# Kernel tuning notes

Hardware: AMD Instinct MI355X
Metric: run time of the kernel (lower is better)

## Reference

```python
import jax, jax.numpy as jnp
import numpy as np

N = 100000   # total nodes
E = 600000   # total edges
B = 50       # graphs in batch
F = 40       # functions per graph (guaranteed by construction)
NPG = N // B # nodes per graph
TF = B * F   # total functions
D0 = 64; H = 128; C = 2
INTER_STEPS = 2


def _seg_mean(x, ids, n):
    s = jax.ops.segment_sum(x, ids, num_segments=n)
    c = jax.ops.segment_sum(jnp.ones((ids.shape[0], 1), x.dtype), ids, num_segments=n)
    return s / jnp.maximum(c, 1.0)


def _enc_edge(h, Ws, Wn, b, src, dst):
    # 2-layer message-passing encoder: h = relu(W_self h + W_nbr mean_{j->i} h_j + b)
    for l in range(2):
        agg = _seg_mean(h[src], dst, h.shape[0])
        h = jax.nn.relu(h @ Ws[l] + agg @ Wn[l] + b[l])
    return h


def _enc_plain(h, Ws, b):
    # encoder on a scale with empty edge set: neighbor term is zero
    for l in range(2):
        h = jax.nn.relu(h @ Ws[l] + b[l])
    return h


def _forward(x0, Wp, bp, e0in_Ws, e0in_Wn, e0in_b, e1in_Ws, e1in_b, e2in_Ws, e2in_b,
             enc0_Ws, enc0_Wn, enc0_b, enc1_Ws, enc1_b, enc2_Ws, enc2_b,
             A0, A1, A2, U0, U1, D1, D2, ib0, ib1, ib2, H1, hb1, H2, hb2,
             edge_index, b0, assign0_local):
    src, dst = edge_index[0], edge_index[1]
    # every graph has exactly F functions, so cumsum offsets reduce to b0*F
    assign0 = assign0_local + b0 * F
    assign1 = jnp.arange(TF, dtype=jnp.int32) // F
    h0 = jax.nn.relu(x0 @ Wp + bp)  # dropout = identity at eval
    h1 = jnp.zeros((TF, H), x0.dtype)
    h2 = jnp.zeros((B, H), x0.dtype)
    h0 = _enc_edge(h0, e0in_Ws, e0in_Wn, e0in_b, src, dst)
    h1 = _enc_plain(h1, e1in_Ws, e1in_b)
    h2 = _enc_plain(h2, e2in_Ws, e2in_b)
    for _ in range(INTER_STEPS):
        # inter-scale fusion: pool up (scatter-mean), broadcast down (gather)
        p01 = _seg_mean(h0, assign0, TF)   # node -> function
        p12 = _seg_mean(h1, assign1, B)    # function -> graph
        n0 = jax.nn.relu(h0 @ A0 + h1[assign0] @ D1 + ib0)
        n1 = jax.nn.relu(h1 @ A1 + p01 @ U0 + h2[assign1] @ D2 + ib1)
        n2 = jax.nn.relu(h2 @ A2 + p12 @ U1 + ib2)
        h0, h1, h2 = n0, n1, n2
        h0 = _enc_edge(h0, enc0_Ws, enc0_Wn, enc0_b, src, dst)
        h1 = _enc_plain(h1, enc1_Ws, enc1_b)
        h2 = _enc_plain(h2, enc2_Ws, enc2_b)
    g0 = _seg_mean(h0, b0, B)        # global_mean_pool over nodes
    g1 = _seg_mean(h1, assign1, B)   # mean over functions per graph
    g = jnp.concatenate([g0, g1, h2], axis=-1)  # [B, 3H]
    return jax.nn.relu(g @ H1 + hb1) @ H2 + hb2


def setup_inputs() -> dict:
    key = jax.random.key(0)
    ks = iter(jax.random.split(key, 64))
    def W(*shape):
        return jax.random.normal(next(ks), shape, dtype=jnp.float32) * 0.05
    inp = {}
    inp["x0"] = jax.random.normal(next(ks), (N, D0), dtype=jnp.float32)
    inp["edge_index"] = jax.random.randint(next(ks), (2, E), 0, N, dtype=jnp.int32)
    inp["b0"] = (jnp.arange(N, dtype=jnp.int32) // NPG)            # sorted graph ids
    inp["assign0_local"] = (jnp.arange(N, dtype=jnp.int32) % NPG) % F  # all F ids per graph
    inp["Wp"] = W(D0, H); inp["bp"] = jnp.zeros((H,), jnp.float32)
    for name in ["e0in", "enc0"]:
        inp[name + "_Ws"] = W(2, H, H); inp[name + "_Wn"] = W(2, H, H)
        inp[name + "_b"] = jnp.zeros((2, H), jnp.float32)
    for name in ["e1in", "e2in", "enc1", "enc2"]:
        inp[name + "_Ws"] = W(2, H, H)
        inp[name + "_b"] = jnp.zeros((2, H), jnp.float32)
    for nm in ["A0", "A1", "A2", "U0", "U1", "D1", "D2"]:
        inp[nm] = W(H, H)
    for nm in ["ib0", "ib1", "ib2"]:
        inp[nm] = jnp.zeros((H,), jnp.float32)
    inp["H1"] = W(3 * H, H); inp["hb1"] = jnp.zeros((H,), jnp.float32)
    inp["H2"] = W(H, C); inp["hb2"] = jnp.zeros((C,), jnp.float32)
    return inp


def reference(x0, edge_index, b0, assign0_local, Wp, bp,
              e0in_Ws, e0in_Wn, e0in_b, e1in_Ws, e1in_b, e2in_Ws, e2in_b,
              enc0_Ws, enc0_Wn, enc0_b, enc1_Ws, enc1_b, enc2_Ws, enc2_b,
              A0, A1, A2, U0, U1, D1, D2, ib0, ib1, ib2, H1, hb1, H2, hb2):
    return _forward(x0, Wp, bp, e0in_Ws, e0in_Wn, e0in_b, e1in_Ws, e1in_b,
                    e2in_Ws, e2in_b, enc0_Ws, enc0_Wn, enc0_b, enc1_Ws, enc1_b,
                    enc2_Ws, enc2_b, A0, A1, A2, U0, U1, D1, D2, ib0, ib1, ib2,
                    H1, hb1, H2, hb2, edge_index, b0, assign0_local)
```

## Files before the change

kernel.cpp:

```cpp
#include <hip/hip_runtime.h>

namespace {

constexpr int N   = 100000;
constexpr int E   = 600000;
constexpr int B   = 50;
constexpr int F   = 40;
constexpr int TF  = B * F;
constexpr int D0  = 64;
constexpr int H   = 128;
constexpr int C   = 2;

typedef __attribute__((ext_vector_type(8))) __bf16 bf16x8;
typedef __attribute__((ext_vector_type(8))) unsigned short us8;
typedef __attribute__((ext_vector_type(4))) float f32x4;

__device__ __forceinline__ float asf(unsigned u) { return __uint_as_float(u); }
__device__ __forceinline__ unsigned bfr(float x) {
  unsigned u = __float_as_uint(x);
  return (u + 0x7FFFu + ((u >> 16) & 1u)) >> 16;
}

__device__ __forceinline__ void glds16(const void* g, void* l) {
  __builtin_amdgcn_global_load_lds(
      (const __attribute__((address_space(1))) unsigned*)g,
      (__attribute__((address_space(3))) unsigned*)l, 16, 0, 0);
}


__global__ void hist_edges(const int* __restrict__ dst, int* __restrict__ deg) {
  int e = blockIdx.x * 256 + threadIdx.x;
  if (e < E) atomicAdd(&deg[dst[e]], 1);
}

__global__ void hist_nodes(const int* __restrict__ b0, const int* __restrict__ a0l,
                           int* __restrict__ cnt1, int* __restrict__ assign0) {
  __shared__ int lh[TF];
  int t = threadIdx.x;
  for (int j = t; j < TF; j += 256) lh[j] = 0;
  __syncthreads();
  int i = blockIdx.x * 256 + t;
  if (i < N) {
    int g = b0[i];
    int a = g * F + a0l[i];
    assign0[i] = a;
    atomicAdd(&lh[a], 1);
  }
  __syncthreads();
  for (int j = t; j < TF; j += 256) {
    int c = lh[j];
    if (c) atomicAdd(&cnt1[j], c);
  }
}

__global__ void scan1(const int* __restrict__ cnt, int* __restrict__ offs,
                      int* __restrict__ part) {
  __shared__ int lds[256];
  int t = threadIdx.x;
  int base = blockIdx.x * 1024 + t * 4;
  int v[4];
#pragma unroll
  for (int j = 0; j < 4; ++j) v[j] = (base + j < N) ? cnt[base + j] : 0;
  int s = v[0] + v[1] + v[2] + v[3];
  lds[t] = s;
  __syncthreads();
  for (int off = 1; off < 256; off <<= 1) {
    int x = (t >= off) ? lds[t - off] : 0;
    __syncthreads();
    lds[t] += x;
    __syncthreads();
  }
  int ex = lds[t] - s;
  if (t == 255) part[blockIdx.x] = lds[255];
  int run = ex;
#pragma unroll
  for (int j = 0; j < 4; ++j) {
    if (base + j < N) offs[base + j] = run;
    run += v[j];
  }
}

__global__ void scan2(const int* __restrict__ part, int* __restrict__ partEx, int nb) {
  __shared__ int lds[128];
  int t = threadIdx.x;
  int s = (t < nb) ? part[t] : 0;
  lds[t] = s;
  __syncthreads();
  for (int off = 1; off < 128; off <<= 1) {
    int x = (t >= off) ? lds[t - off] : 0;
    __syncthreads();
    lds[t] += x;
    __syncthreads();
  }
  partEx[t] = lds[t] - s;
}

__global__ void scan3(int* __restrict__ offs, const int* __restrict__ partEx,
                      const int* __restrict__ deg, float* __restrict__ rdeg,
                      const int* __restrict__ cnt1, float* __restrict__ rdeg1,
                      float* __restrict__ rdegB) {
  int i = blockIdx.x * 256 + threadIdx.x;
  if (i < N) {
    offs[i] += partEx[i >> 10];
    rdeg[i] = 1.0f / fmaxf((float)deg[i], 1.0f);
    if (i == 0) offs[N] = E;
    if (i < TF) rdeg1[i] = 1.0f / fmaxf((float)cnt1[i], 1.0f);
    if (i < B) {
      int s = 0;
      for (int f = 0; f < F; ++f) s += cnt1[i * F + f];
      rdegB[i] = 1.0f / fmaxf((float)s, 1.0f);
    }
  }
}

__global__ void scatter_k(const int* __restrict__ src, const int* __restrict__ dst,
                          const int* __restrict__ offs, int* __restrict__ cursor,
                          int* __restrict__ srcS) {
  int e = blockIdx.x * 256 + threadIdx.x;
  if (e < E) {
    int d = dst[e];
    int pos = offs[d] + atomicAdd(&cursor[d], 1);
    srcS[pos] = src[e];
  }
}

struct WPtrs { const float* w[19]; };
__global__ void conv_w(WPtrs wp, unsigned short* __restrict__ wt) {
  int i = blockIdx.x >> 6;
  int e = (blockIdx.x & 63) * 256 + threadIdx.x;
  int k = e >> 7, c = e & 127;
  float x = wp.w[i][e];
  unsigned h = bfr(x);
  unsigned l = bfr(x - asf(h << 16));
  int cs = (c & 7) * 16 + (c >> 3);
  size_t o = (size_t)i * 32768 + (k >> 5) * 4096 + cs * 32 + (k & 31);
  wt[o] = (unsigned short)h;
  wt[o + 16384] = (unsigned short)l;
}

__global__ void conv_wp(const float* __restrict__ w, unsigned short* __restrict__ wt) {
  int e = blockIdx.x * 256 + threadIdx.x;
  int k = e >> 7, c = e & 127;
  float x = w[e];
  unsigned h = bfr(x);
  unsigned l = bfr(x - asf(h << 16));
  int cs = (c & 7) * 16 + (c >> 3);
  size_t o = (size_t)(k >> 5) * 4096 + cs * 32 + (k & 31);
  wt[o] = (unsigned short)h;
  wt[o + 8192] = (unsigned short)l;
}

__global__ void x0split(const float* __restrict__ x0, unsigned short* __restrict__ xs) {
  int i = blockIdx.x * 256 + threadIdx.x;
  if (i >= N * D0) return;
  int row = i >> 6, c = i & 63;
  float x = x0[i];
  unsigned h = bfr(x);
  unsigned l = bfr(x - asf(h << 16));
  xs[(size_t)row * 128 + c] = (unsigned short)h;
  xs[(size_t)row * 128 + 64 + c] = (unsigned short)l;
}

__global__ void warm_k(const uint4* __restrict__ w, unsigned* __restrict__ dummy) {
  uint4 v = w[blockIdx.x * 256 + threadIdx.x];
  unsigned x = v.x ^ v.y ^ v.z ^ v.w;
  if (x == 0xDEADBEEFu) dummy[0] = 1u;
}

__global__ void agg_k(const unsigned short* __restrict__ Act,
                      const int* __restrict__ offs, const int* __restrict__ srcS,
                      const float* __restrict__ rdeg, unsigned short* __restrict__ Out) {
  int wid = blockIdx.x * 4 + (threadIdx.x >> 6);
  int lane = threadIdx.x & 63;
  if (wid >= N) return;
  int o0 = offs[wid], o1 = offs[wid + 1];
  float s0 = 0.f, s1 = 0.f;
  int e = o0;
  for (; e + 3 < o1; e += 4) {
    unsigned v0 = *(const unsigned*)(Act + (size_t)srcS[e] * 256 + lane * 2);
    unsigned v1 = *(const unsigned*)(Act + (size_t)srcS[e + 1] * 256 + lane * 2);
    unsigned v2 = *(const unsigned*)(Act + (size_t)srcS[e + 2] * 256 + lane * 2);
    unsigned v3 = *(const unsigned*)(Act + (size_t)srcS[e + 3] * 256 + lane * 2);
    s0 += asf(v0 << 16) + asf(v1 << 16) + asf(v2 << 16) + asf(v3 << 16);
    s1 += asf(v0 & 0xFFFF0000u) + asf(v1 & 0xFFFF0000u) +
          asf(v2 & 0xFFFF0000u) + asf(v3 & 0xFFFF0000u);
  }
  for (; e < o1; ++e) {
    unsigned v0 = *(const unsigned*)(Act + (size_t)srcS[e] * 256 + lane * 2);
    s0 += asf(v0 << 16);
    s1 += asf(v0 & 0xFFFF0000u);
  }
  float sc = rdeg[wid];
  unsigned h0 = bfr(s0 * sc), h1 = bfr(s1 * sc);
  *(unsigned*)(Out + (size_t)wid * 256 + lane * 2) = h0 | (h1 << 16);
}

template <int KD, bool AGG, bool GATH, bool BLO = true>
__global__ __launch_bounds__(256, 3)
void mgemm(const unsigned short* __restrict__ Ai, const unsigned short* __restrict__ W1,
           const unsigned short* __restrict__ Bi, const unsigned short* __restrict__ W2,
           const float* __restrict__ Gt, const int* __restrict__ Gidx,
           const float* __restrict__ bias, unsigned short* __restrict__ Oi, int n) {
  __shared__ unsigned short wlds[2][2][4096];
  constexpr int KS = KD / 32;
  constexpr int NS = (AGG ? 2 : 1) * KS;
  constexpr int KLO = KD * 128;
  constexpr int ARS = 2 * KD;
  const int t = threadIdx.x, wv = t >> 6, ln = t & 63;
  const int row0 = blockIdx.x * 128 + wv * 32;
  const int lm = ln & 15, kg = ln >> 4;
  int ar0 = row0 + lm, ar1 = row0 + 16 + lm;
  if (ar0 >= n) ar0 = 0;
  if (ar1 >= n) ar1 = 0;
  const size_t a0off = (size_t)ar0 * ARS, a1off = (size_t)ar1 * ARS;

  f32x4 acc[2][8];
#pragma unroll
  for (int i = 0; i < 2; ++i)
#pragma unroll
    for (int j = 0; j < 8; ++j) acc[i][j] = (f32x4){0.f, 0.f, 0.f, 0.f};

  uint4 sA, sB, sC, sD;
  bf16x8 a0h[2], a0l[2], a1h[2], a1l[2];

  auto ldst = [&](int s) {
    const unsigned short* W = (AGG && s >= KS) ? W2 : W1;
    const unsigned short* ph = W + (s & (KS - 1)) * 4096;
    sA = *(const uint4*)(ph + t * 8);
    sB = *(const uint4*)(ph + 2048 + t * 8);
    sC = *(const uint4*)(ph + KLO + t * 8);
    sD = *(const uint4*)(ph + KLO + 2048 + t * 8);
  };
  auto wrst = [&](int buf) {
    *(uint4*)&wlds[buf][0][t * 8] = sA;
    *(uint4*)&wlds[buf][0][2048 + t * 8] = sB;
    *(uint4*)&wlds[buf][1][t * 8] = sC;
    *(uint4*)&wlds[buf][1][2048 + t * 8] = sD;
  };
  auto loadA = [&](int s, int w) {
    const bool bpass = AGG && (s >= KS);
    const unsigned short* X = bpass ? Bi : Ai;
    int kk = (s & (KS - 1)) * 32 + kg * 8;
    a0h[w] = *(const bf16x8*)(X + a0off + kk);
    a1h[w] = *(const bf16x8*)(X + a1off + kk);
    if (!bpass || BLO) {
      a0l[w] = *(const bf16x8*)(X + a0off + KD + kk);
      a1l[w] = *(const bf16x8*)(X + a1off + KD + kk);
    }
  };

  ldst(0); wrst(0); loadA(0, 0);
  __syncthreads();

#pragma unroll
  for (int s = 0; s < NS; ++s) {
    const int buf = s & 1;
    const bool uselo = !(AGG && (s >= KS)) || BLO;
    if (s + 1 < NS) { ldst(s + 1); loadA(s + 1, buf ^ 1); }
#pragma unroll
    for (int nf = 0; nf < 8; ++nf) {
      const int wo = (nf * 16 + lm) * 32 + kg * 8;
      bf16x8 wh = *(const bf16x8*)&wlds[buf][0][wo];
      bf16x8 wl = *(const bf16x8*)&wlds[buf][1][wo];
      acc[0][nf] = __builtin_amdgcn_mfma_f32_16x16x32_bf16(a0h[buf], wh, acc[0][nf], 0, 0, 0);
      acc[0][nf] = __builtin_amdgcn_mfma_f32_16x16x32_bf16(a0h[buf], wl, acc[0][nf], 0, 0, 0);
      if (uselo)
        acc[0][nf] = __builtin_amdgcn_mfma_f32_16x16x32_bf16(a0l[buf], wh, acc[0][nf], 0, 0, 0);
      acc[1][nf] = __builtin_amdgcn_mfma_f32_16x16x32_bf16(a1h[buf], wh, acc[1][nf], 0, 0, 0);
      acc[1][nf] = __builtin_amdgcn_mfma_f32_16x16x32_bf16(a1h[buf], wl, acc[1][nf], 0, 0, 0);
      if (uselo)
        acc[1][nf] = __builtin_amdgcn_mfma_f32_16x16x32_bf16(a1l[buf], wh, acc[1][nf], 0, 0, 0);
    }
    if (s + 1 < NS) wrst(buf ^ 1);
    __syncthreads();
  }

  float4 bq0 = *(const float4*)&bias[lm * 8];
  float4 bq1 = *(const float4*)&bias[lm * 8 + 4];
  float bsv[8] = {bq0.x, bq0.y, bq0.z, bq0.w, bq1.x, bq1.y, bq1.z, bq1.w};
#pragma unroll
  for (int mf = 0; mf < 2; ++mf)
#pragma unroll
    for (int rr = 0; rr < 4; ++rr) {
      int row = row0 + mf * 16 + kg * 4 + rr;
      if (row >= n) continue;
      float gvv[8];
      if (GATH) {
        const float* grow = Gt + (size_t)Gidx[row] * H + lm * 8;
        float4 g0 = *(const float4*)grow;
        float4 g1 = *(const float4*)(grow + 4);
        gvv[0] = g0.x; gvv[1] = g0.y; gvv[2] = g0.z; gvv[3] = g0.w;
        gvv[4] = g1.x; gvv[5] = g1.y; gvv[6] = g1.z; gvv[7] = g1.w;
      }
      us8 hv, lv;
#pragma unroll
      for (int nf = 0; nf < 8; ++nf) {
        float v = acc[mf][nf][rr] + bsv[nf];
        if (GATH) v += gvv[nf];
        v = fmaxf(v, 0.f);
        unsigned h = bfr(v);
        hv[nf] = (unsigned short)h;
        lv[nf] = (unsigned short)bfr(v - asf(h << 16));
      }
      *(us8*)(Oi + (size_t)row * 256 + lm * 8) = hv;
      *(us8*)(Oi + (size_t)row * 256 + 128 + lm * 8) = lv;
    }
}

template <bool ISH1>
__global__ __launch_bounds__(512)
void fused_chain(const unsigned short* __restrict__ Ai,
                 const float* __restrict__ P, const float* __restrict__ pscale,
                 const float* __restrict__ Gt,
                 const unsigned short* __restrict__ Wd,
                 const unsigned short* __restrict__ Wa,
                 const unsigned short* __restrict__ Wu,
                 const unsigned short* __restrict__ We0,
                 const unsigned short* __restrict__ We1,
                 const float* __restrict__ bn, const float* __restrict__ be0,
                 const float* __restrict__ be1,
                 float* __restrict__ outD, unsigned short* __restrict__ Ao,
                 float* __restrict__ outF, int n) {
  __shared__ unsigned short act[128 * 256];
  __shared__ unsigned short wl[2][16384];
  const int t = threadIdx.x, wv = t >> 6, ln = t & 63;
  const int lm = ln & 15, kg = ln >> 4;
  const int rbase = blockIdx.x * 128 + wv * 16;
  const int lbase = wv * 16;
  int ar = rbase + lm;
  if (ar >= n) ar = 0;

  const unsigned short* mats[5] = {Wd, Wa, Wu, We0, We1};

  f32x4 acc[8];
  auto zacc = [&]() {
#pragma unroll
    for (int nf = 0; nf < 8; ++nf) acc[nf] = (f32x4){0.f, 0.f, 0.f, 0.f};
  };

  auto ldwl = [&](int s, int b) {
    const unsigned short* hi = mats[s >> 1] + (s & 1) * 8192;
    const unsigned short* lo = mats[s >> 1] + 16384 + (s & 1) * 8192;
    const int wo = wv * 1024;
    const int lo8 = ln * 8;
#pragma unroll
    for (int j = 0; j < 2; ++j) {
      glds16(hi + wo + j * 512 + lo8, &wl[b][wo + j * 512]);
      glds16(lo + wo + j * 512 + lo8, &wl[b][8192 + wo + j * 512]);
    }
  };
  auto ldact = [&]() {
    const unsigned short* src = Ai + (size_t)blockIdx.x * (128 * 256);
    const int base = wv * 4096;
    const int lo8 = ln * 8;
#pragma unroll
    for (int j = 0; j < 8; ++j)
      glds16(src + base + j * 512 + lo8, &act[base + j * 512]);
  };

  auto donf = [&](int b, int ksl, bf16x8 ah, bf16x8 al) {
#pragma unroll
    for (int nf = 0; nf < 8; ++nf) {
      const int wo = ksl * 4096 + (nf * 16 + lm) * 32 + kg * 8;
      bf16x8 wh = *(const bf16x8*)&wl[b][wo];
      bf16x8 wq = *(const bf16x8*)&wl[b][8192 + wo];
      acc[nf] = __builtin_amdgcn_mfma_f32_16x16x32_bf16(ah, wh, acc[nf], 0, 0, 0);
      acc[nf] = __builtin_amdgcn_mfma_f32_16x16x32_bf16(ah, wq, acc[nf], 0, 0, 0);
      acc[nf] = __builtin_amdgcn_mfma_f32_16x16x32_bf16(al, wh, acc[nf], 0, 0, 0);
    }
  };

  auto epiAct = [&](const float* bias, bool gath) {
    float4 b0 = *(const float4*)&bias[lm * 8];
    float4 b1 = *(const float4*)&bias[lm * 8 + 4];
    float bv[8] = {b0.x, b0.y, b0.z, b0.w, b1.x, b1.y, b1.z, b1.w};
#pragma unroll
    for (int rr = 0; rr < 4; ++rr) {
      int rl = lbase + kg * 4 + rr;
      int rg = rbase + kg * 4 + rr;
      float gv[8] = {0.f, 0.f, 0.f, 0.f, 0.f, 0.f, 0.f, 0.f};
      if (ISH1 && gath && rg < n) {
        const float* grow = Gt + (size_t)(rg / F) * H + lm * 8;
        float4 g0 = *(const float4*)grow;
        float4 g1 = *(const float4*)(grow + 4);
        gv[0] = g0.x; gv[1] = g0.y; gv[2] = g0.z; gv[3] = g0.w;
        gv[4] = g1.x; gv[5] = g1.y; gv[6] = g1.z; gv[7] = g1.w;
      }
      us8 hv, lv;
#pragma unroll
      for (int nf = 0; nf < 8; ++nf) {
        float v = acc[nf][rr] + bv[nf] + gv[nf];
        v = fmaxf(v, 0.f);
        unsigned h = bfr(v);
        hv[nf] = (unsigned short)h;
        lv[nf] = (unsigned short)bfr(v - asf(h << 16));
      }
      *(us8*)&act[rl * 256 + lm * 8] = hv;
      *(us8*)&act[rl * 256 + 128 + lm * 8] = lv;
    }
  };

  ldact();
  ldwl(0, 0);
  __syncthreads();
  ldwl(1, 1);

#pragma unroll
  for (int s = 0; s < 10; ++s) {
    const int b = s & 1;
    if (s == 0 || s == 2 || s == 6 || s == 8) zacc();
    const int m = s >> 1;
#pragma unroll
    for (int ksl = 0; ksl < 2; ++ksl) {
      const int ks = (s & 1) * 2 + ksl;
      bf16x8 ah, al;
      if (m == 2) {
        const float* pp = P + (size_t)ar * H + ks * 32 + kg * 8;
        float4 f0 = *(const float4*)pp;
        float4 f1 = *(const float4*)(pp + 4);
        if (ISH1) {
          float sc = pscale[ar];
          f0.x *= sc; f0.y *= sc; f0.z *= sc; f0.w *= sc;
          f1.x *= sc; f1.y *= sc; f1.z *= sc; f1.w *= sc;
        }
        float fv[8] = {f0.x, f0.y, f0.z, f0.w, f1.x, f1.y, f1.z, f1.w};
        us8 h8, l8;
#pragma unroll
        for (int j = 0; j < 8; ++j) {
          unsigned h = bfr(fv[j]);
          h8[j] = (unsigned short)h;
          l8[j] = (unsigned short)bfr(fv[j] - asf(h << 16));
        }
        ah = __builtin_bit_cast(bf16x8, h8);
        al = __builtin_bit_cast(bf16x8, l8);
      } else {
        int rl = lbase + lm;
        ah = *(const bf16x8*)&act[rl * 256 + ks * 32 + kg * 8];
        al = *(const bf16x8*)&act[rl * 256 + 128 + ks * 32 + kg * 8];
      }
      donf(b, ksl, ah, al);
    }
    if (s == 1) {
#pragma unroll
      for (int rr = 0; rr < 4; ++rr) {
        int rg = rbase + kg * 4 + rr;
        if (rg < n) {
          float* op = outD + (size_t)rg * H + lm * 8;
          *(float4*)op = make_float4(acc[0][rr], acc[1][rr], acc[2][rr], acc[3][rr]);
          *(float4*)(op + 4) = make_float4(acc[4][rr], acc[5][rr], acc[6][rr], acc[7][rr]);
        }
      }
    }
    if (s == 5) epiAct(bn, true);
    if (s == 7) epiAct(be0, false);
    if (s == 9) {
      float4 b0 = *(const float4*)&be1[lm * 8];
      float4 b1 = *(const float4*)&be1[lm * 8 + 4];
      float bv[8] = {b0.x, b0.y, b0.z, b0.w, b1.x, b1.y, b1.z, b1.w};
#pragma unroll
      for (int rr = 0; rr < 4; ++rr) {
        int rg = rbase + kg * 4 + rr;
        if (rg >= n) continue;
        us8 hv, lv;
        float fv[8];
#pragma unroll
        for (int nf = 0; nf < 8; ++nf) {
          float v = fmaxf(acc[nf][rr] + bv[nf], 0.f);
          fv[nf] = v;
          unsigned h = bfr(v);
          hv[nf] = (unsigned short)h;
          lv[nf] = (unsigned short)bfr(v - asf(h << 16));
        }
        *(us8*)(Ao + (size_t)rg * 256 + lm * 8) = hv;
        *(us8*)(Ao + (size_t)rg * 256 + 128 + lm * 8) = lv;
        if (outF) {
          float* op = outF + (size_t)rg * H + lm * 8;
          *(float4*)op = make_float4(fv[0], fv[1], fv[2], fv[3]);
          *(float4*)(op + 4) = make_float4(fv[4], fv[5], fv[6], fv[7]);
        }
      }
    }
    if (s + 1 < 10) {
      __syncthreads();
      if (s + 2 < 10) ldwl(s + 2, b);
    }
  }
}

__global__ void init_bcast(const float* __restrict__ Ws1, const float* __restrict__ b1,
                           const float* __restrict__ Ws2, const float* __restrict__ b2,
                           unsigned short* __restrict__ h1i, unsigned short* __restrict__ h2i) {
  __shared__ float z0[128];
  int t = threadIdx.x;
  bool ish2 = (blockIdx.x == 20);
  const float* W = ish2 ? Ws2 : Ws1;
  const float* bb = ish2 ? b2 : b1;
  z0[t] = fmaxf(bb[t], 0.f);
  __syncthreads();
  float s = bb[128 + t];
  for (int k = 0; k < 128; ++k) s += z0[k] * W[16384 + k * 128 + t];
  s = fmaxf(s, 0.f);
  unsigned h = bfr(s);
  unsigned l = bfr(s - asf(h << 16));
  if (ish2) {
    for (int r = 0; r < B; ++r) {
      h2i[(size_t)r * 256 + t] = (unsigned short)h;
      h2i[(size_t)r * 256 + 128 + t] = (unsigned short)l;
    }
  } else {
    int r0 = blockIdx.x * 100;
    for (int r = 0; r < 100; ++r) {
      h1i[(size_t)(r0 + r) * 256 + t] = (unsigned short)h;
      h1i[(size_t)(r0 + r) * 256 + 128 + t] = (unsigned short)l;
    }
  }
}

__global__ void pool_p01(const unsigned short* __restrict__ Act,
                         const int* __restrict__ a0l, const int* __restrict__ b0,
                         float* __restrict__ p01s) {
  __shared__ float acc[F][H];
  int t = threadIdx.x;
#pragma unroll
  for (int f = 0; f < F; ++f) acc[f][t] = 0.f;
  int rowbase = blockIdx.x * 250;
  for (int i = 0; i < 250; ++i) {
    size_t r = (size_t)(rowbase + i) * 256 + t;
    acc[a0l[rowbase + i]][t] += asf((unsigned)Act[r] << 16) + asf((unsigned)Act[r + 128] << 16);
  }
  int g = b0[rowbase];
#pragma unroll
  for (int f = 0; f < F; ++f)
    atomicAdd(&p01s[((size_t)(g * F + f)) * H + t], acc[f][t]);
}

__global__ void pool_g0(const unsigned short* __restrict__ Act,
                        const int* __restrict__ b0, float* __restrict__ g0s) {
  int t = threadIdx.x;
  int rowbase = blockIdx.x * 250;
  float a = 0.f;
  for (int i = 0; i < 250; ++i) {
    size_t r = (size_t)(rowbase + i) * 256 + t;
    a += asf((unsigned)Act[r] << 16) + asf((unsigned)Act[r + 128] << 16);
  }
  atomicAdd(&g0s[(size_t)b0[rowbase] * H + t], a);
}

__global__ void mean40i(const unsigned short* __restrict__ Act, float* __restrict__ outp) {
  int t = threadIdx.x, g = blockIdx.x;
  float a = 0.f;
  for (int i = 0; i < F; ++i) {
    size_t r = (size_t)(g * F + i) * 256 + t;
    a += asf((unsigned)Act[r] << 16) + asf((unsigned)Act[r + 128] << 16);
  }
  outp[(size_t)g * H + t] = a * (1.0f / F);
}

__global__ void head_k(const float* __restrict__ g0s, const float* __restrict__ rdegB,
                       const float* __restrict__ g1, const float* __restrict__ h2,
                       const float* __restrict__ W1h, const float* __restrict__ b1h,
                       const float* __restrict__ W2h, const float* __restrict__ b2h,
                       float* __restrict__ out) {
  __shared__ float gv[3 * H];
  __shared__ float z[H];
  int b = blockIdx.x, t = threadIdx.x;
  gv[t] = g0s[(size_t)b * H + t] * rdegB[b];
  gv[H + t] = g1[(size_t)b * H + t];
  gv[2 * H + t] = h2[(size_t)b * H + t];
  __syncthreads();
  float s = b1h[t];
  for (int k = 0; k < 3 * H; ++k) s += gv[k] * W1h[k * H + t];
  z[t] = fmaxf(s, 0.f);
  __syncthreads();
  if (t < C) {
    float o = b2h[t];
    for (int k = 0; k < H; ++k) o += z[k] * W2h[k * C + t];
    out[b * C + t] = o;
  }
}

}

extern "C" void kernel_launch(void* const* d_in, const int* in_sizes, int n_in,
                              void* d_out, int out_size, void* d_ws, size_t ws_size,
                              hipStream_t stream) {
  (void)in_sizes; (void)n_in; (void)out_size; (void)ws_size;
  const float* x0   = (const float*)d_in[0];
  const int*   ei   = (const int*)d_in[1];
  const int*   src  = ei;
  const int*   dst  = ei + E;
  const int*   b0   = (const int*)d_in[2];
  const int*   a0l  = (const int*)d_in[3];
  const float* Wp   = (const float*)d_in[4];
  const float* bp   = (const float*)d_in[5];
  const float* e0in_Ws = (const float*)d_in[6];
  const float* e0in_Wn = (const float*)d_in[7];
  const float* e0in_b  = (const float*)d_in[8];
  const float* enc0_Ws = (const float*)d_in[9];
  const float* enc0_Wn = (const float*)d_in[10];
  const float* enc0_b  = (const float*)d_in[11];
  const float* e1in_Ws = (const float*)d_in[12];
  const float* e1in_b  = (const float*)d_in[13];
  const float* e2in_Ws = (const float*)d_in[14];
  const float* e2in_b  = (const float*)d_in[15];
  const float* enc1_Ws = (const float*)d_in[16];
  const float* enc1_b  = (const float*)d_in[17];
  const float* enc2_Ws = (const float*)d_in[18];
  const float* enc2_b  = (const float*)d_in[19];
  const float* A0 = (const float*)d_in[20];
  const float* A1 = (const float*)d_in[21];
  const float* A2 = (const float*)d_in[22];
  const float* U0 = (const float*)d_in[23];
  const float* U1 = (const float*)d_in[24];
  const float* D1 = (const float*)d_in[25];
  const float* D2 = (const float*)d_in[26];
  const float* ib0 = (const float*)d_in[27];
  const float* ib1 = (const float*)d_in[28];
  const float* ib2 = (const float*)d_in[29];
  const float* H1w = (const float*)d_in[30];
  const float* hb1 = (const float*)d_in[31];
  const float* H2w = (const float*)d_in[32];
  const float* hb2 = (const float*)d_in[33];
  float* out = (float*)d_out;

  char* p = (char*)d_ws;
  auto carve = [&](size_t bytes) {
    char* r = p;
    p += (bytes + 255) & ~(size_t)255;
    return r;
  };
  char* z0 = p;
  int*   deg    = (int*)carve((size_t)N * 4);
  int*   cursor = (int*)carve((size_t)N * 4);
  int*   cnt1   = (int*)carve((size_t)TF * 4);
  float* g0s    = (float*)carve((size_t)B * H * 4);
  size_t zbytes = (size_t)(p - z0);
  unsigned short* h0i  = (unsigned short*)carve((size_t)N * 256 * 2);
  unsigned short* aggi = (unsigned short*)carve((size_t)N * 256 * 2);
  unsigned short* h1a  = (unsigned short*)carve((size_t)2048 * 256 * 2);
  unsigned short* h2ai = (unsigned short*)carve((size_t)128 * 256 * 2);
  float* h1d  = (float*)carve((size_t)TF * H * 4);
  float* h2d  = (float*)carve((size_t)64 * H * 4);
  float* h2f  = (float*)carve((size_t)B * H * 4);
  float* p01s = (float*)carve((size_t)TF * H * 4);
  float* p12  = (float*)carve((size_t)64 * H * 4);
  float* g1   = (float*)carve((size_t)B * H * 4);
  float* rdeg = (float*)carve((size_t)N * 4);
  float* rdeg1 = (float*)carve((size_t)TF * 4);
  float* rdegB = (float*)carve(64 * 4);
  int* offs    = (int*)carve((size_t)(N + 64) * 4);
  int* srcS    = (int*)carve((size_t)E * 4);
  int* part    = (int*)carve(128 * 4);
  int* partEx  = (int*)carve(128 * 4);
  int* assign0 = (int*)carve((size_t)N * 4);
  unsigned short* wt  = (unsigned short*)carve((size_t)19 * 32768 * 2);
  unsigned short* wt9 = (unsigned short*)carve((size_t)16384 * 2);
  unsigned short* xs  = aggi;

  const int HH = H * H;
  const int MG = (N + 127) / 128;

  hipMemsetAsync(z0, 0, zbytes, stream);
  hist_edges<<<(E + 255) / 256, 256, 0, stream>>>(dst, deg);
  hist_nodes<<<(N + 255) / 256, 256, 0, stream>>>(b0, a0l, cnt1, assign0);
  const int nb1 = (N + 1023) / 1024;
  scan1<<<nb1, 256, 0, stream>>>(deg, offs, part);
  scan2<<<1, 128, 0, stream>>>(part, partEx, nb1);
  scan3<<<(N + 255) / 256, 256, 0, stream>>>(offs, partEx, deg, rdeg, cnt1, rdeg1,
                                             rdegB);
  scatter_k<<<(E + 255) / 256, 256, 0, stream>>>(src, dst, offs, cursor, srcS);
  {
    WPtrs wp;
    wp.w[0] = e0in_Ws;      wp.w[1] = e0in_Ws + HH;
    wp.w[2] = e0in_Wn;      wp.w[3] = e0in_Wn + HH;
    wp.w[4] = enc0_Ws;      wp.w[5] = enc0_Ws + HH;
    wp.w[6] = enc0_Wn;      wp.w[7] = enc0_Wn + HH;
    wp.w[8] = A0;
    wp.w[9] = D1;           wp.w[10] = A1;
    wp.w[11] = U0;          wp.w[12] = enc1_Ws;   wp.w[13] = enc1_Ws + HH;
    wp.w[14] = D2;          wp.w[15] = A2;
    wp.w[16] = U1;          wp.w[17] = enc2_Ws;   wp.w[18] = enc2_Ws + HH;
    conv_w<<<19 * 64, 256, 0, stream>>>(wp, wt);
  }
  conv_wp<<<32, 256, 0, stream>>>(Wp, wt9);
  x0split<<<(N * D0 + 255) / 256, 256, 0, stream>>>(x0, xs);

  mgemm<64, false, false><<<MG, 256, 0, stream>>>(
      xs, wt9, nullptr, nullptr, nullptr, nullptr, bp, h0i, N);

  auto encEdgeM = [&](int wsIdx, int wnIdx, const float* barr) {
    for (int l = 0; l < 2; ++l) {
      agg_k<<<N / 4, 256, 0, stream>>>(h0i, offs, srcS, rdeg, aggi);
      mgemm<128, true, false, false><<<MG, 256, 0, stream>>>(
          h0i, wt + (size_t)(wsIdx + l) * 32768, aggi,
          wt + (size_t)(wnIdx + l) * 32768, nullptr, nullptr, barr + l * H, h0i, N);
    }
  };

  encEdgeM(0, 2, e0in_b);
  init_bcast<<<21, 128, 0, stream>>>(e1in_Ws, e1in_b, e2in_Ws, e2in_b, h1a, h2ai);

  for (int step = 0; step < 2; ++step) {
    hipMemsetAsync(p01s, 0, (size_t)TF * H * 4, stream);
    pool_p01<<<400, 128, 0, stream>>>(h0i, a0l, b0, p01s);
    mean40i<<<B, 128, 0, stream>>>(h1a, p12);
    warm_k<<<160, 256, 0, stream>>>((const uint4*)(wt + (size_t)9 * 32768),
                                    (unsigned*)cursor);
    fused_chain<false><<<1, 512, 0, stream>>>(
        h2ai, p12, nullptr, nullptr,
        wt + (size_t)14 * 32768, wt + (size_t)15 * 32768, wt + (size_t)16 * 32768,
        wt + (size_t)17 * 32768, wt + (size_t)18 * 32768,
        ib2, enc2_b, enc2_b + H, h2d, h2ai, h2f, B);
    fused_chain<true><<<16, 512, 0, stream>>>(
        h1a, p01s, rdeg1, h2d,
        wt + (size_t)9 * 32768, wt + (size_t)10 * 32768, wt + (size_t)11 * 32768,
        wt + (size_t)12 * 32768, wt + (size_t)13 * 32768,
        ib1, enc1_b, enc1_b + H, h1d, h1a, nullptr, TF);
    mgemm<128, false, true><<<MG, 256, 0, stream>>>(
        h0i, wt + (size_t)8 * 32768, nullptr, nullptr, h1d, assign0, ib0, h0i, N);
    encEdgeM(4, 6, enc0_b);
  }

  pool_g0<<<400, 128, 0, stream>>>(h0i, b0, g0s);
  mean40i<<<B, 128, 0, stream>>>(h1a, g1);
  head_k<<<B, 128, 0, stream>>>(g0s, rdegB, g1, h2f, H1w, hb1, H2w, hb2, out);
}
```

Baseline: 831.1 us.

## Merge graph-level and function-level fused chains into one launch

The two per-step fused_chain launches (one block for the graph level, 16 blocks for the function level) are replaced by a single 17-block kernel. One block handles the graph-level role and computes h2·D2 for the next step into a double buffer. The first h2·D2 is precomputed by a new small kernel before the loop. This removes the serial dependency and one launch per step so both levels run concurrently. The cost is that the step loops are no longer unrolled and the kernel branches on role.

```diff
diff --git a/kernel.cpp b/kernel.cpp
--- a/kernel.cpp
+++ b/kernel.cpp
@@ -307,30 +307,91 @@
     }
 }
 
-template <bool ISH1>
 __global__ __launch_bounds__(512)
-void fused_chain(const unsigned short* __restrict__ Ai,
-                 const float* __restrict__ P, const float* __restrict__ pscale,
-                 const float* __restrict__ Gt,
-                 const unsigned short* __restrict__ Wd,
-                 const unsigned short* __restrict__ Wa,
-                 const unsigned short* __restrict__ Wu,
-                 const unsigned short* __restrict__ We0,
-                 const unsigned short* __restrict__ We1,
-                 const float* __restrict__ bn, const float* __restrict__ be0,
-                 const float* __restrict__ be1,
-                 float* __restrict__ outD, unsigned short* __restrict__ Ao,
-                 float* __restrict__ outF, int n) {
+void h2d_k(const unsigned short* __restrict__ h2ai, const unsigned short* __restrict__ Wm,
+           float* __restrict__ h2d) {
+  __shared__ unsigned short wl[32768];
+  const int t = threadIdx.x, wv = t >> 6, ln = t & 63;
+  const int lm = ln & 15, kg = ln >> 4;
+  const int lo8 = ln * 8;
+#pragma unroll
+  for (int j = 0; j < 8; ++j)
+    glds16(Wm + (wv * 8 + j) * 512 + lo8, &wl[(wv * 8 + j) * 512]);
+  __syncthreads();
+  if (wv >= 4) return;
+  int ar = wv * 16 + lm;
+  if (ar >= B) ar = 0;
+  f32x4 acc[8];
+#pragma unroll
+  for (int nf = 0; nf < 8; ++nf) acc[nf] = (f32x4){0.f, 0.f, 0.f, 0.f};
+#pragma unroll
+  for (int ks = 0; ks < 4; ++ks) {
+    bf16x8 ah = *(const bf16x8*)(h2ai + (size_t)ar * 256 + ks * 32 + kg * 8);
+    bf16x8 al = *(const bf16x8*)(h2ai + (size_t)ar * 256 + 128 + ks * 32 + kg * 8);
+#pragma unroll
+    for (int nf = 0; nf < 8; ++nf) {
+      const int wo = ks * 4096 + (nf * 16 + lm) * 32 + kg * 8;
+      bf16x8 wh = *(const bf16x8*)&wl[wo];
+      bf16x8 wq = *(const bf16x8*)&wl[16384 + wo];
+      acc[nf] = __builtin_amdgcn_mfma_f32_16x16x32_bf16(ah, wh, acc[nf], 0, 0, 0);
+      acc[nf] = __builtin_amdgcn_mfma_f32_16x16x32_bf16(ah, wq, acc[nf], 0, 0, 0);
+      acc[nf] = __builtin_amdgcn_mfma_f32_16x16x32_bf16(al, wh, acc[nf], 0, 0, 0);
+    }
+  }
+#pragma unroll
+  for (int rr = 0; rr < 4; ++rr) {
+    int rg = wv * 16 + kg * 4 + rr;
+    if (rg < B) {
+      float* op = h2d + (size_t)rg * H + lm * 8;
+      *(float4*)op = make_float4(acc[0][rr], acc[1][rr], acc[2][rr], acc[3][rr]);
+      *(float4*)(op + 4) = make_float4(acc[4][rr], acc[5][rr], acc[6][rr], acc[7][rr]);
+    }
+  }
+}
+
+struct ChainArgs {
+  const unsigned short* Ai1; const unsigned short* Ai2;
+  const float* P1; const float* P2; const float* ps1;
+  const float* Gt1;
+  const unsigned short* w1[5];
+  const unsigned short* w2[6];
+  const float *bn1, *be01, *be11, *bn2, *be02, *be12;
+  float* outD1;
+  unsigned short* Ao1; unsigned short* Ao2;
+  float* outF2;
+  float* outDn2;
+  int n1, n2;
+};
+
+__global__ __launch_bounds__(512)
+void fused_chain2(ChainArgs a) {
   __shared__ unsigned short act[128 * 256];
   __shared__ unsigned short wl[2][16384];
+  const bool role = (blockIdx.x == 16);
   const int t = threadIdx.x, wv = t >> 6, ln = t & 63;
   const int lm = ln & 15, kg = ln >> 4;
-  const int rbase = blockIdx.x * 128 + wv * 16;
+  const int rbase = (role ? 0 : blockIdx.x * 128) + wv * 16;
   const int lbase = wv * 16;
+  const int n = role ? a.n2 : a.n1;
+  const int nst = role ? 12 : 10;
+  const unsigned short* Ai = role ? a.Ai2 : a.Ai1;
+  const float* P = role ? a.P2 : a.P1;
+  unsigned short* Ao = role ? a.Ao2 : a.Ao1;
+  const float* bn  = role ? a.bn2 : a.bn1;
+  const float* be0 = role ? a.be02 : a.be01;
+  const float* be1 = role ? a.be12 : a.be11;
   int ar = rbase + lm;
   if (ar >= n) ar = 0;
 
-  const unsigned short* mats[5] = {Wd, Wa, Wu, We0, We1};
+  const unsigned short* mats[6];
+  if (role) {
+#pragma unroll
+    for (int i = 0; i < 6; ++i) mats[i] = a.w2[i];
+  } else {
+#pragma unroll
+    for (int i = 0; i < 5; ++i) mats[i] = a.w1[i];
+    mats[5] = a.w1[0];
+  }
 
   f32x4 acc[8];
   auto zacc = [&]() {
@@ -350,7 +411,7 @@
     }
   };
   auto ldact = [&]() {
-    const unsigned short* src = Ai + (size_t)blockIdx.x * (128 * 256);
+    const unsigned short* src = Ai + (size_t)(role ? 0 : blockIdx.x) * (128 * 256);
     const int base = wv * 4096;
     const int lo8 = ln * 8;
 #pragma unroll
@@ -379,8 +440,8 @@
       int rl = lbase + kg * 4 + rr;
       int rg = rbase + kg * 4 + rr;
       float gv[8] = {0.f, 0.f, 0.f, 0.f, 0.f, 0.f, 0.f, 0.f};
-      if (ISH1 && gath && rg < n) {
-        const float* grow = Gt + (size_t)(rg / F) * H + lm * 8;
+      if (!role && gath && rg < n) {
+        const float* grow = a.Gt1 + (size_t)(rg / F) * H + lm * 8;
         float4 g0 = *(const float4*)grow;
         float4 g1 = *(const float4*)(grow + 4);
         gv[0] = g0.x; gv[1] = g0.y; gv[2] = g0.z; gv[3] = g0.w;
@@ -405,12 +466,10 @@
   __syncthreads();
   ldwl(1, 1);
 
-#pragma unroll
-  for (int s = 0; s < 10; ++s) {
+  for (int s = 0; s < nst; ++s) {
     const int b = s & 1;
-    if (s == 0 || s == 2 || s == 6 || s == 8) zacc();
+    if ((s & 1) == 0 && s != 4) zacc();
     const int m = s >> 1;
-#pragma unroll
     for (int ksl = 0; ksl < 2; ++ksl) {
       const int ks = (s & 1) * 2 + ksl;
       bf16x8 ah, al;
@@ -418,8 +477,8 @@
         const float* pp = P + (size_t)ar * H + ks * 32 + kg * 8;
         float4 f0 = *(const float4*)pp;
         float4 f1 = *(const float4*)(pp + 4);
-        if (ISH1) {
-          float sc = pscale[ar];
+        if (!role) {
+          float sc = a.ps1[ar];
           f0.x *= sc; f0.y *= sc; f0.z *= sc; f0.w *= sc;
           f1.x *= sc; f1.y *= sc; f1.z *= sc; f1.w *= sc;
         }
@@ -440,12 +499,12 @@
       }
       donf(b, ksl, ah, al);
     }
-    if (s == 1) {
+    if (s == 1 && !role) {
 #pragma unroll
       for (int rr = 0; rr < 4; ++rr) {
         int rg = rbase + kg * 4 + rr;
         if (rg < n) {
-          float* op = outD + (size_t)rg * H + lm * 8;
+          float* op = a.outD1 + (size_t)rg * H + lm * 8;
           *(float4*)op = make_float4(acc[0][rr], acc[1][rr], acc[2][rr], acc[3][rr]);
           *(float4*)(op + 4) = make_float4(acc[4][rr], acc[5][rr], acc[6][rr], acc[7][rr]);
         }
@@ -459,8 +518,8 @@
       float bv[8] = {b0.x, b0.y, b0.z, b0.w, b1.x, b1.y, b1.z, b1.w};
 #pragma unroll
       for (int rr = 0; rr < 4; ++rr) {
+        int rl = lbase + kg * 4 + rr;
         int rg = rbase + kg * 4 + rr;
-        if (rg >= n) continue;
         us8 hv, lv;
         float fv[8];
 #pragma unroll
@@ -471,18 +530,35 @@
           hv[nf] = (unsigned short)h;
           lv[nf] = (unsigned short)bfr(v - asf(h << 16));
         }
-        *(us8*)(Ao + (size_t)rg * 256 + lm * 8) = hv;
-        *(us8*)(Ao + (size_t)rg * 256 + 128 + lm * 8) = lv;
-        if (outF) {
-          float* op = outF + (size_t)rg * H + lm * 8;
-          *(float4*)op = make_float4(fv[0], fv[1], fv[2], fv[3]);
-          *(float4*)(op + 4) = make_float4(fv[4], fv[5], fv[6], fv[7]);
+        if (role) {
+          *(us8*)&act[rl * 256 + lm * 8] = hv;
+          *(us8*)&act[rl * 256 + 128 + lm * 8] = lv;
+        }
+        if (rg < n) {
+          *(us8*)(Ao + (size_t)rg * 256 + lm * 8) = hv;
+          *(us8*)(Ao + (size_t)rg * 256 + 128 + lm * 8) = lv;
+          if (role) {
+            float* op = a.outF2 + (size_t)rg * H + lm * 8;
+            *(float4*)op = make_float4(fv[0], fv[1], fv[2], fv[3]);
+            *(float4*)(op + 4) = make_float4(fv[4], fv[5], fv[6], fv[7]);
+          }
         }
       }
     }
-    if (s + 1 < 10) {
+    if (s == 11) {
+#pragma unroll
+      for (int rr = 0; rr < 4; ++rr) {
+        int rg = rbase + kg * 4 + rr;
+        if (rg < n) {
+          float* op = a.outDn2 + (size_t)rg * H + lm * 8;
+          *(float4*)op = make_float4(acc[0][rr], acc[1][rr], acc[2][rr], acc[3][rr]);
+          *(float4*)(op + 4) = make_float4(acc[4][rr], acc[5][rr], acc[6][rr], acc[7][rr]);
+        }
+      }
+    }
+    if (s + 1 < nst) {
       __syncthreads();
-      if (s + 2 < 10) ldwl(s + 2, b);
+      if (s + 2 < nst) ldwl(s + 2, b);
     }
   }
 }
@@ -640,7 +716,8 @@
   unsigned short* h1a  = (unsigned short*)carve((size_t)2048 * 256 * 2);
   unsigned short* h2ai = (unsigned short*)carve((size_t)128 * 256 * 2);
   float* h1d  = (float*)carve((size_t)TF * H * 4);
-  float* h2d  = (float*)carve((size_t)64 * H * 4);
+  float* h2dA = (float*)carve((size_t)64 * H * 4);
+  float* h2dB = (float*)carve((size_t)64 * H * 4);
   float* h2f  = (float*)carve((size_t)B * H * 4);
   float* p01s = (float*)carve((size_t)TF * H * 4);
   float* p12  = (float*)carve((size_t)64 * H * 4);
@@ -699,23 +776,35 @@
 
   encEdgeM(0, 2, e0in_b);
   init_bcast<<<21, 128, 0, stream>>>(e1in_Ws, e1in_b, e2in_Ws, e2in_b, h1a, h2ai);
-
+  h2d_k<<<1, 512, 0, stream>>>(h2ai, wt + (size_t)14 * 32768, h2dA);
+
+  float* h2dbuf[2] = {h2dA, h2dB};
   for (int step = 0; step < 2; ++step) {
     hipMemsetAsync(p01s, 0, (size_t)TF * H * 4, stream);
     pool_p01<<<400, 128, 0, stream>>>(h0i, a0l, b0, p01s);
     mean40i<<<B, 128, 0, stream>>>(h1a, p12);
     warm_k<<<160, 256, 0, stream>>>((const uint4*)(wt + (size_t)9 * 32768),
                                     (unsigned*)cursor);
-    fused_chain<false><<<1, 512, 0, stream>>>(
-        h2ai, p12, nullptr, nullptr,
-        wt + (size_t)14 * 32768, wt + (size_t)15 * 32768, wt + (size_t)16 * 32768,
-        wt + (size_t)17 * 32768, wt + (size_t)18 * 32768,
-        ib2, enc2_b, enc2_b + H, h2d, h2ai, h2f, B);
-    fused_chain<true><<<16, 512, 0, stream>>>(
-        h1a, p01s, rdeg1, h2d,
-        wt + (size_t)9 * 32768, wt + (size_t)10 * 32768, wt + (size_t)11 * 32768,
-        wt + (size_t)12 * 32768, wt + (size_t)13 * 32768,
-        ib1, enc1_b, enc1_b + H, h1d, h1a, nullptr, TF);
+    {
+      ChainArgs ca;
+      ca.Ai1 = h1a;  ca.Ai2 = h2ai;
+      ca.P1 = p01s;  ca.P2 = p12;  ca.ps1 = rdeg1;
+      ca.Gt1 = h2dbuf[step & 1];
+      ca.w1[0] = wt + (size_t)9 * 32768;  ca.w1[1] = wt + (size_t)10 * 32768;
+      ca.w1[2] = wt + (size_t)11 * 32768; ca.w1[3] = wt + (size_t)12 * 32768;
+      ca.w1[4] = wt + (size_t)13 * 32768;
+      ca.w2[0] = wt + (size_t)14 * 32768; ca.w2[1] = wt + (size_t)15 * 32768;
+      ca.w2[2] = wt + (size_t)16 * 32768; ca.w2[3] = wt + (size_t)17 * 32768;
+      ca.w2[4] = wt + (size_t)18 * 32768; ca.w2[5] = wt + (size_t)14 * 32768;
+      ca.bn1 = ib1;  ca.be01 = enc1_b;  ca.be11 = enc1_b + H;
+      ca.bn2 = ib2;  ca.be02 = enc2_b;  ca.be12 = enc2_b + H;
+      ca.outD1 = h1d;
+      ca.Ao1 = h1a;  ca.Ao2 = h2ai;
+      ca.outF2 = h2f;
+      ca.outDn2 = h2dbuf[(step + 1) & 1];
+      ca.n1 = TF;  ca.n2 = B;
+      fused_chain2<<<17, 512, 0, stream>>>(ca);
+    }
     mgemm<128, false, true><<<MG, 256, 0, stream>>>(
         h0i, wt + (size_t)8 * 32768, nullptr, nullptr, h1d, assign0, ib0, h0i, N);
     encEdgeM(4, 6, enc0_b);
```

New measurement: 777.8 us (median of 2 runs). 6.4% less time.
